# Optimization experiments

Measured on AMD Instinct MI355X. Metric: run time of the kernel, lower is better.

The kernel has to match this reference:

```python
import jax, jax.numpy as jnp
import numpy as np

BATCH, SEQ, D = 128, 256, 64


def setup_inputs() -> dict:
    key = jax.random.key(0)
    k1, k2, k3 = jax.random.split(key, 3)
    eye = jnp.eye(D, dtype=jnp.float32)
    return {
        "x": jax.random.normal(k1, (BATCH, D), dtype=jnp.float32),
        "U_t": jax.random.normal(k2, (BATCH, SEQ, D), dtype=jnp.float32),
        "Y_t": jax.random.normal(k3, (BATCH, SEQ, D), dtype=jnp.float32),
        # learnable params, 'identity' init per module
        "F_mat": eye,
        "B_mat": eye,
        "H": eye,
        "LQ": jnp.tril(eye),
        "LR": jnp.tril(eye),
    }


def _kalman(x, U_t, Y_t, F_mat, B_mat, H, LQ, LR):
    d = x.shape[-1]
    bsz = x.shape[0]
    Q = LQ @ LQ.T                      # [D,D] process noise cov
    R = LR @ LR.T                      # [D,D] measurement noise cov
    I = jnp.eye(d, dtype=x.dtype)
    P0 = jnp.broadcast_to(I, (bsz, d, d))

    def step(carry, inp):
        x_prev, P = carry              # [B,D], [B,D,D]
        u, y = inp                     # [B,D], [B,D,D]
        x_pred = x_prev @ F_mat.T + u @ B_mat.T
        P_pred = F_mat @ P @ F_mat.T + Q            # broadcasts [D,D]@[B,D,D]
        S = H @ P_pred @ H.T + R                    # [B,D,D]
        S_inv = jnp.linalg.inv(S)
        K = P_pred @ (H.T @ S_inv)                  # Kalman gain [B,D,D]
        innov = y - x_pred @ H.T                    # [B,D]
        # matches torch: (innov.unsqueeze(1) @ K).squeeze(1)
        x_new = x_pred + jnp.einsum('bd,bde->be', innov, K)
        IKH = I - K @ H
        P_new = IKH @ P_pred @ jnp.swapaxes(IKH, -1, -2) \
              + K @ R @ jnp.swapaxes(K, -1, -2)
        P_new = 0.5 * (P_new + jnp.swapaxes(P_new, -1, -2))  # symmetrize
        return (x_new, P_new), (x_new, P_new)

    inputs = (jnp.swapaxes(U_t, 0, 1), jnp.swapaxes(Y_t, 0, 1))  # [S,B,D]
    _, (preds, covs) = jax.lax.scan(step, (x, P0), inputs)
    # prediction [B,S,D], covariance [B,S,D,D]
    return jnp.swapaxes(preds, 0, 1), jnp.swapaxes(covs, 0, 1)


def reference(x, U_t, Y_t, F_mat, B_mat, H, LQ, LR):
    return _kalman(x, U_t, Y_t, F_mat, B_mat, H, LQ, LR)
```

## Files before the change

kernel.cpp:

```cpp
#include <hip/hip_runtime.h>

#define BATCH 128
#define SEQ   256

#define WS_K  16
#define WS_A  (16 + SEQ * 4096)
#define WS_BP (WS_A + 4096)
#define WS_KS (WS_BP + 4096)

typedef unsigned short u16;
typedef float  f32x4v __attribute__((ext_vector_type(4)));
typedef __bf16 bf16x8 __attribute__((ext_vector_type(8)));
typedef unsigned short u16x8 __attribute__((ext_vector_type(8)));

struct Acc { f32x4v t[2][2]; };

__device__ __forceinline__ u16 bf16hi(float x) {
  unsigned u = __float_as_uint(x);
  return (u16)((u + 0x7fffu + ((u >> 16) & 1u)) >> 16);
}
__device__ __forceinline__ float bf16f(u16 h) {
  return __uint_as_float(((unsigned)h) << 16);
}

__device__ __forceinline__ int swadr(int a, int c) {
  return a * 64 + ((c ^ (a & 7)) << 3);
}

__device__ __forceinline__ bf16x8 frag(const u16* M, int strip, int kb, int q, int ln) {
  return *(const bf16x8*)(M + swadr(strip * 16 + ln, kb * 4 + q));
}

__device__ __forceinline__ void mm(const u16* As, const u16* Bs, Acc& acc,
                                   int R, int Cb, int q, int ln) {
#pragma unroll
  for (int kb = 0; kb < 2; ++kb) {
    bf16x8 ah[2], al[2], bh[2], bl[2];
#pragma unroll
    for (int i = 0; i < 2; ++i) {
      ah[i] = frag(As,        2 * R  + i, kb, q, ln);
      al[i] = frag(As + 4096, 2 * R  + i, kb, q, ln);
      bh[i] = frag(Bs,        2 * Cb + i, kb, q, ln);
      bl[i] = frag(Bs + 4096, 2 * Cb + i, kb, q, ln);
    }
#pragma unroll
    for (int i = 0; i < 2; ++i)
#pragma unroll
      for (int j = 0; j < 2; ++j) {
        acc.t[i][j] = __builtin_amdgcn_mfma_f32_16x16x32_bf16(ah[i], bh[j], acc.t[i][j], 0, 0, 0);
        acc.t[i][j] = __builtin_amdgcn_mfma_f32_16x16x32_bf16(ah[i], bl[j], acc.t[i][j], 0, 0, 0);
        acc.t[i][j] = __builtin_amdgcn_mfma_f32_16x16x32_bf16(al[i], bh[j], acc.t[i][j], 0, 0, 0);
      }
  }
}

__device__ __forceinline__ Acc accZero() {
  Acc a;
#pragma unroll
  for (int i = 0; i < 2; ++i)
#pragma unroll
    for (int j = 0; j < 2; ++j) {
      f32x4v z; z.x = 0.f; z.y = 0.f; z.z = 0.f; z.w = 0.f;
      a.t[i][j] = z;
    }
  return a;
}

__device__ __forceinline__ void storeC(float* dst, const Acc& a, int R, int Cb, int q, int ln) {
#pragma unroll
  for (int i = 0; i < 2; ++i)
#pragma unroll
    for (int j = 0; j < 2; ++j)
#pragma unroll
      for (int k = 0; k < 4; ++k)
        dst[(32 * R + 16 * i + 4 * q + k) * 64 + 32 * Cb + 16 * j + ln] = a.t[i][j][k];
}

__device__ __forceinline__ void emit16(const float* v, int row, int cb, u16* Rs, u16* Ts) {
  u16 h[16], lo[16];
#pragma unroll
  for (int e = 0; e < 16; ++e) {
    h[e] = bf16hi(v[e]);
    lo[e] = bf16hi(v[e] - bf16f(h[e]));
  }
  if (Rs) {
#pragma unroll
    for (int c = 0; c < 2; ++c) {
      u16x8 vh, vl;
#pragma unroll
      for (int e = 0; e < 8; ++e) { vh[e] = h[8 * c + e]; vl[e] = lo[8 * c + e]; }
      const int ad = swadr(row, (cb >> 3) + c);
      *(u16x8*)(Rs + ad) = vh;
      *(u16x8*)(Rs + 4096 + ad) = vl;
    }
  }
  if (Ts) {
    const int rc = row >> 3, rr = row & 7;
#pragma unroll
    for (int e = 0; e < 16; ++e) {
      const int a = cb + e;
      const int ad = a * 64 + ((rc ^ (a & 7)) << 3) + rr;
      Ts[ad] = h[e];
      Ts[4096 + ad] = lo[e];
    }
  }
}

__device__ __forceinline__ void splitsrc(const float* src, u16* Rs, u16* Ts,
                                         int mode, float scale, float dval, int tid) {
  const int row = tid >> 2, cb = (tid & 3) << 4;
  float v[16];
#pragma unroll
  for (int m = 0; m < 4; ++m) {
    f32x4v x = *(const f32x4v*)(src + row * 64 + cb + 4 * m);
    v[4 * m] = x.x; v[4 * m + 1] = x.y; v[4 * m + 2] = x.z; v[4 * m + 3] = x.w;
  }
  if (mode == 1) {
#pragma unroll
    for (int e = 0; e < 16; ++e) v[e] *= scale;
  } else if (mode == 2) {
#pragma unroll
    for (int e = 0; e < 16; ++e) v[e] = (((cb + e) == row) ? dval : 0.f) - v[e];
  }
  emit16(v, row, cb, Rs, Ts);
}

__device__ __forceinline__ float redmax(float v, float* red, int tid) {
#pragma unroll
  for (int off = 32; off > 0; off >>= 1) v = fmaxf(v, __shfl_xor(v, off));
  if ((tid & 63) == 0) red[300 + (tid >> 6)] = v;
  __syncthreads();
  float m = fmaxf(fmaxf(red[300], red[301]), fmaxf(red[302], red[303]));
  __syncthreads();
  return m;
}

__device__ __forceinline__ float dot4(float4 a, float4 b, float acc) {
  return fmaf(a.x, b.x, fmaf(a.y, b.y, fmaf(a.z, b.z, fmaf(a.w, b.w, acc))));
}

__global__ void __launch_bounds__(256, 1)
k1_riccati(const float* __restrict__ Fg, const float* __restrict__ Bg,
           const float* __restrict__ Hg, const float* __restrict__ LQg,
           const float* __restrict__ LRg, float* __restrict__ ws,
           float* __restrict__ covs) {
  __shared__ __align__(16) u16 smb[7 * 8192];
  __shared__ __align__(16) float Mf32[4096];
  __shared__ __align__(16) float Ppf32[4096];
  __shared__ __align__(16) float red[308];

  const int tid = threadIdx.x;
  const int l = tid & 63, w = tid >> 6, q = l >> 4, ln = l & 15;
  const int R = w >> 1, Cb = w & 1;

  {
    const int row = tid >> 2, cb = (tid & 3) << 4;
    float od = 0.f;
    const float* mats[5] = {Fg, Bg, Hg, LQg, LRg};
#pragma unroll
    for (int mi = 0; mi < 5; ++mi) {
      const float* M = mats[mi];
#pragma unroll
      for (int m = 0; m < 4; ++m) {
        f32x4v x = *(const f32x4v*)(M + row * 64 + cb + 4 * m);
        const int j0c = cb + 4 * m;
        if (j0c + 0 != row) od = fmaxf(od, fabsf(x.x));
        if (j0c + 1 != row) od = fmaxf(od, fabsf(x.y));
        if (j0c + 2 != row) od = fmaxf(od, fabsf(x.z));
        if (j0c + 3 != row) od = fmaxf(od, fabsf(x.w));
      }
    }
    const float odall = redmax(od, red, tid);
    if (odall == 0.f) {
      if (tid < 64) {
        const int e = tid;
        const float f = Fg[e * 65], b = Bg[e * 65], h = Hg[e * 65];
        const float lq = LQg[e * 65], lr = LRg[e * 65];
        const float qv = lq * lq, rv = lr * lr;
        float p = 1.f, kprev = 0.f, kcur = 0.f, om = 1.f;
        int tstar = SEQ - 1;
        for (int t = 0; t < SEQ; ++t) {
          const float pp = f * p * f + qv;
          const float s = h * pp * h + rv;
          const float k = pp * h / s;
          const float kh = k * h;
          const float omv = 1.f - kh;
          const float pn = omv * omv * pp + k * k * rv;
          float* Kt = ws + WS_K + (size_t)t * 4096 + e * 64;
          float* Ct = covs + (size_t)t * 4096 + e * 64;
          f32x4v z; z.x = 0.f; z.y = 0.f; z.z = 0.f; z.w = 0.f;
#pragma unroll
          for (int m = 0; m < 16; ++m) {
            *(f32x4v*)(Kt + 4 * m) = z;
            *(f32x4v*)(Ct + 4 * m) = z;
          }
          Kt[e] = k;
          Ct[e] = pn;
          float dk = (t == 0) ? 1e9f : fabsf(k - kprev);
#pragma unroll
          for (int off = 32; off > 0; off >>= 1) dk = fmaxf(dk, __shfl_xor(dk, off));
          p = pn; kprev = k; kcur = k; om = omv;
          if (dk < 1e-3f) { tstar = t; break; }
        }
        {
          const float astar = om * f, bpv = om * b;
          float* Ar = ws + WS_A + e * 64;
          float* Bp = ws + WS_BP + e * 64;
          float* Ks = ws + WS_KS + e * 64;
          f32x4v z; z.x = 0.f; z.y = 0.f; z.z = 0.f; z.w = 0.f;
#pragma unroll
          for (int m = 0; m < 16; ++m) {
            *(f32x4v*)(Ar + 4 * m) = z;
            *(f32x4v*)(Bp + 4 * m) = z;
            *(f32x4v*)(Ks + 4 * m) = z;
          }
          Ar[e] = astar; Bp[e] = bpv; Ks[e] = kcur;
          const float a2 = astar * astar, a4 = a2 * a2, a8 = a4 * a4;
          float a16 = fabsf(a8 * a8);
#pragma unroll
          for (int off = 32; off > 0; off >>= 1) a16 = fmaxf(a16, __shfl_xor(a16, off));
          if (e == 0) {
            ((int*)ws)[0] = tstar;
            ((int*)ws)[1] = (tstar <= 16 && a16 < 1e-5f) ? 1 : 0;
          }
        }
      }
      return;
    }
  }

  u16* SF = smb;
  u16* SH = smb + 8192;
  u16* SX = smb + 2 * 8192;
  u16* S1 = smb + 3 * 8192;
  u16* S2 = smb + 4 * 8192;
  u16* S3 = smb + 5 * 8192;
  u16* S4 = smb + 6 * 8192;

  splitsrc(Fg, SF, nullptr, 0, 0, 0, tid);
  splitsrc(Hg, SH, nullptr, 0, 0, 0, tid);
  splitsrc(LQg, S1, nullptr, 0, 0, 0, tid);
  __syncthreads();
  Acc qacc = accZero(); mm(S1, S1, qacc, R, Cb, q, ln);
  __syncthreads();
  splitsrc(LRg, S1, nullptr, 0, 0, 0, tid);
  __syncthreads();
  Acc racc = accZero(); mm(S1, S1, racc, R, Cb, q, ln);
  __syncthreads();
  {
    const int row = tid >> 2, cb = (tid & 3) << 4;
    float v[16];
#pragma unroll
    for (int e = 0; e < 16; ++e) v[e] = ((cb + e) == row) ? 1.f : 0.f;
    emit16(v, row, cb, S4, nullptr);
  }
  __syncthreads();

  int tstar = SEQ - 1;
  for (int t = 0; t < SEQ; ++t) {
    const u16* Wsrc = SF;
    if (t > 0) {
      Acc a = accZero(); mm(SF, S4, a, R, Cb, q, ln);
      storeC(Mf32, a, R, Cb, q, ln);
      __syncthreads();
      splitsrc(Mf32, S1, nullptr, 0, 0, 0, tid);
      __syncthreads();
      Wsrc = S1;
    }
    {
      Acc a = qacc; mm(Wsrc, SF, a, R, Cb, q, ln);
      storeC(Ppf32, a, R, Cb, q, ln);
      __syncthreads();
      splitsrc(Ppf32, S2, nullptr, 0, 0, 0, tid);
      __syncthreads();
    }
    {
      Acc a = accZero(); mm(SH, S2, a, R, Cb, q, ln);
      storeC(Mf32, a, R, Cb, q, ln);
      __syncthreads();
      splitsrc(Mf32, S3, S4, 0, 0, 0, tid);
      __syncthreads();
    }
    {
      Acc a = racc; mm(S3, SH, a, R, Cb, q, ln);
      storeC(Mf32, a, R, Cb, q, ln);
      __syncthreads();
      if (t == 0) {
        const int col = tid & 63, grp = tid >> 6;
        float s = 0.f;
        for (int r2 = grp * 16; r2 < grp * 16 + 16; ++r2) s += fabsf(Mf32[r2 * 64 + col]);
        red[tid] = s;
        __syncthreads();
        if (tid < 64) {
          float cs = red[tid] + red[64 + tid] + red[128 + tid] + red[192 + tid];
#pragma unroll
          for (int off = 32; off > 0; off >>= 1) cs = fmaxf(cs, __shfl_xor(cs, off));
          if (tid == 0) red[256] = 1.f / (cs * cs);
        }
        __syncthreads();
        const float sc = red[256];
        splitsrc(Mf32, SX, nullptr, 1, sc, 0, tid);
        __syncthreads();
      }
      splitsrc(Mf32, S2, nullptr, 0, 0, 0, tid);
      __syncthreads();
    }
    const int cap = (t == 0) ? 40 : 4;
    for (int it = 0; it < cap; ++it) {
      Acc e_ = accZero(); mm(S2, SX, e_, R, Cb, q, ln);
      float r = 0.f;
#pragma unroll
      for (int i = 0; i < 2; ++i)
#pragma unroll
        for (int j = 0; j < 2; ++j)
#pragma unroll
          for (int k = 0; k < 4; ++k) {
            const int gr = 32 * R + 16 * i + 4 * q + k;
            const int gc = 32 * Cb + 16 * j + ln;
            r = fmaxf(r, fabsf(e_.t[i][j][k] - ((gr == gc) ? 1.f : 0.f)));
          }
      const float rall = redmax(r, red, tid);
      if (rall < 5e-4f) break;
      storeC(Mf32, e_, R, Cb, q, ln);
      __syncthreads();
      splitsrc(Mf32, nullptr, S1, 2, 0, 2.0f, tid);
      __syncthreads();
      Acc x2 = accZero(); mm(SX, S1, x2, R, Cb, q, ln);
      storeC(Mf32, x2, R, Cb, q, ln);
      __syncthreads();
      splitsrc(Mf32, SX, nullptr, 0, 0, 0, tid);
      __syncthreads();
      if (rall * rall < 1e-4f) break;
    }
    __syncthreads();
    float dk;
    {
      Acc a = accZero(); mm(SX, S4, a, R, Cb, q, ln);
      storeC(Mf32, a, R, Cb, q, ln);
      __syncthreads();
      const int row = tid >> 2, cb = (tid & 3) << 4;
      float v[16]; float dmax = (t == 0) ? 1e9f : 0.f;
      float* wrow = ws + WS_K + (size_t)t * 4096 + row * 64 + cb;
#pragma unroll
      for (int m = 0; m < 4; ++m) {
        f32x4v x = *(const f32x4v*)(Mf32 + row * 64 + cb + 4 * m);
        v[4 * m] = x.x; v[4 * m + 1] = x.y; v[4 * m + 2] = x.z; v[4 * m + 3] = x.w;
        *(f32x4v*)(wrow + 4 * m) = x;
      }
      if (t > 0) {
        const float* prow = wrow - 4096;
#pragma unroll
        for (int m = 0; m < 4; ++m) {
          f32x4v p = *(const f32x4v*)(prow + 4 * m);
          dmax = fmaxf(dmax, fmaxf(fmaxf(fabsf(v[4 * m] - p.x), fabsf(v[4 * m + 1] - p.y)),
                                   fmaxf(fabsf(v[4 * m + 2] - p.z), fabsf(v[4 * m + 3] - p.w))));
        }
      }
      emit16(v, row, cb, nullptr, S1);
      dk = redmax(dmax, red, tid);
    }
    {
      Acc a = accZero(); mm(S1, S4, a, R, Cb, q, ln);
      storeC(Mf32, a, R, Cb, q, ln);
      __syncthreads();
      const int row = tid >> 2, cb = (tid & 3) << 4;
      float pv[16];
#pragma unroll
      for (int m = 0; m < 4; ++m) {
        f32x4v mij = *(const f32x4v*)(Mf32 + row * 64 + cb + 4 * m);
        f32x4v pp  = *(const f32x4v*)(Ppf32 + row * 64 + cb + 4 * m);
        pv[4 * m]     = pp.x - 0.5f * (mij.x + Mf32[(cb + 4 * m + 0) * 64 + row]);
        pv[4 * m + 1] = pp.y - 0.5f * (mij.y + Mf32[(cb + 4 * m + 1) * 64 + row]);
        pv[4 * m + 2] = pp.z - 0.5f * (mij.z + Mf32[(cb + 4 * m + 2) * 64 + row]);
        pv[4 * m + 3] = pp.w - 0.5f * (mij.w + Mf32[(cb + 4 * m + 3) * 64 + row]);
      }
      float* crow = covs + (size_t)t * 4096 + row * 64 + cb;
#pragma unroll
      for (int m = 0; m < 4; ++m) {
        f32x4v o; o.x = pv[4 * m]; o.y = pv[4 * m + 1]; o.z = pv[4 * m + 2]; o.w = pv[4 * m + 3];
        *(f32x4v*)(crow + 4 * m) = o;
      }
      emit16(pv, row, cb, S4, nullptr);
      __syncthreads();
    }
    if (dk < 1e-3f) { tstar = t; break; }
  }

  {
    Acc a = accZero(); mm(S1, SH, a, R, Cb, q, ln);
    storeC(Mf32, a, R, Cb, q, ln);
    __syncthreads();
    splitsrc(Mf32, S2, nullptr, 2, 0, 1.0f, tid);
    __syncthreads();
  }
  splitsrc(Fg, nullptr, S3, 0, 0, 0, tid);
  __syncthreads();
  {
    Acc a = accZero(); mm(S2, S3, a, R, Cb, q, ln);
    storeC(Mf32, a, R, Cb, q, ln);
#pragma unroll
    for (int i = 0; i < 2; ++i)
#pragma unroll
      for (int j = 0; j < 2; ++j)
#pragma unroll
        for (int k = 0; k < 4; ++k)
          ws[WS_A + (size_t)((32 * R + 16 * i + 4 * q + k) * 64 + 32 * Cb + 16 * j + ln)] = a.t[i][j][k];
    __syncthreads();
    splitsrc(Mf32, S1, S4, 0, 0, 0, tid);
    __syncthreads();
  }
  splitsrc(Bg, nullptr, S3, 0, 0, 0, tid);
  __syncthreads();
  {
    Acc a = accZero(); mm(S2, S3, a, R, Cb, q, ln);
#pragma unroll
    for (int i = 0; i < 2; ++i)
#pragma unroll
      for (int j = 0; j < 2; ++j)
#pragma unroll
        for (int k = 0; k < 4; ++k)
          ws[WS_BP + (size_t)((32 * R + 16 * i + 4 * q + k) * 64 + 32 * Cb + 16 * j + ln)] = a.t[i][j][k];
  }
  {
    const int row = tid >> 2, cb = (tid & 3) << 4;
    const float* srcr = ws + WS_K + (size_t)tstar * 4096 + row * 64 + cb;
    float* dstr = ws + WS_KS + row * 64 + cb;
#pragma unroll
    for (int m = 0; m < 4; ++m) *(f32x4v*)(dstr + 4 * m) = *(const f32x4v*)(srcr + 4 * m);
  }
  __syncthreads();
  {
    Acc a = accZero(); mm(S1, S4, a, R, Cb, q, ln);
    storeC(Mf32, a, R, Cb, q, ln); __syncthreads();
    splitsrc(Mf32, S2, S3, 0, 0, 0, tid); __syncthreads();
  }
  {
    Acc a = accZero(); mm(S2, S3, a, R, Cb, q, ln);
    storeC(Mf32, a, R, Cb, q, ln); __syncthreads();
    splitsrc(Mf32, S1, S4, 0, 0, 0, tid); __syncthreads();
  }
  {
    Acc a = accZero(); mm(S1, S4, a, R, Cb, q, ln);
    storeC(Mf32, a, R, Cb, q, ln); __syncthreads();
    splitsrc(Mf32, S2, S3, 0, 0, 0, tid); __syncthreads();
  }
  {
    Acc a = accZero(); mm(S2, S3, a, R, Cb, q, ln);
    float am = 0.f;
#pragma unroll
    for (int i = 0; i < 2; ++i)
#pragma unroll
      for (int j = 0; j < 2; ++j)
#pragma unroll
        for (int k = 0; k < 4; ++k) am = fmaxf(am, fabsf(a.t[i][j][k]));
    const float amax = redmax(am, red, tid);
    if (tid == 0) {
      ((int*)ws)[0] = tstar;
      ((int*)ws)[1] = (tstar <= 16 && amax < 1e-5f) ? 1 : 0;
    }
  }
}

#define NB2 512
#define NX2 1024

__global__ void __launch_bounds__(256, 4)
k2_fused(const float* __restrict__ x0, const float* __restrict__ U,
         const float* __restrict__ Y, const float* __restrict__ Fg,
         const float* __restrict__ Bg, const float* __restrict__ Hg,
         const float* __restrict__ ws, float* __restrict__ preds,
         float* __restrict__ covs) {
  const int tid = threadIdx.x;
  const int wg = blockIdx.x;
  const int tstar = ((const int*)ws)[0];
  const int flag  = ((const int*)ws)[1];

  if (wg < NB2) {
    const int b = wg >> 2, qt = wg & 3;
    const int s0 = qt << 6;
    const float4* srcInf = (const float4*)(covs + (size_t)tstar * 4096);
    float4 r0 = srcInf[tid], r1 = srcInf[256 + tid];
    float4 r2 = srcInf[512 + tid], r3 = srcInf[768 + tid];
    for (int s = s0; s < s0 + 64; ++s) {
      float4* dst = (float4*)(covs + ((size_t)b * SEQ + s) * 4096);
      if (s <= tstar) {
        if (b == 0) continue;
        const float4* src = (const float4*)(covs + (size_t)s * 4096);
        dst[tid] = src[tid]; dst[256 + tid] = src[256 + tid];
        dst[512 + tid] = src[512 + tid]; dst[768 + tid] = src[768 + tid];
      } else {
        dst[tid] = r0; dst[256 + tid] = r1; dst[512 + tid] = r2; dst[768 + tid] = r3;
      }
    }
  } else {
    const int xw = wg - NB2;
    const int c = xw >> 7, b = xw & 127;
    const int e = tid >> 2, q = tid & 3;
    const int co = q << 4;
    __shared__ __align__(16) float xa[64], xb[64], inn[64], us[2][64], ys[2][64];

    if (c == 0) {
      const int t1 = flag ? 32 : SEQ;
      float4 Fr[4], Br[4], Hr[4], Kr[4];
      {
        const float4* fp = (const float4*)(Fg + e * 64 + co);
        const float4* bp = (const float4*)(Bg + e * 64 + co);
        const float4* hp = (const float4*)(Hg + e * 64 + co);
#pragma unroll
        for (int m = 0; m < 4; ++m) { Fr[m] = fp[m]; Br[m] = bp[m]; Hr[m] = hp[m]; }
      }
      if (tid < 64) xa[tid] = x0[b * 64 + tid];
      int staged = -1;
      for (int t = 0; t < t1; ++t) {
        const int se = (t < tstar) ? t : tstar;
        if (se != staged) {
          const float4* kp = (const float4*)(ws + WS_K + (size_t)se * 4096 + e * 64 + co);
#pragma unroll
          for (int m = 0; m < 4; ++m) Kr[m] = kp[m];
          staged = se;
        }
        if (tid < 64) us[0][tid] = U[((size_t)b * SEQ + t) * 64 + tid];
        else if (tid < 128) ys[0][tid - 64] = Y[((size_t)b * SEQ + t) * 64 + (tid - 64)];
        __syncthreads();
        const float4* xv4 = (const float4*)xa;
        const float4* us4 = (const float4*)us[0];
        float v = 0.f;
#pragma unroll
        for (int m = 0; m < 4; ++m) {
          v = dot4(Fr[m], xv4[q * 4 + m], v);
          v = dot4(Br[m], us4[q * 4 + m], v);
        }
        v += __shfl_xor(v, 1); v += __shfl_xor(v, 2);
        if (q == 0) xb[e] = v;
        __syncthreads();
        const float4* xp4 = (const float4*)xb;
        float wv = 0.f;
#pragma unroll
        for (int m = 0; m < 4; ++m) wv = dot4(Hr[m], xp4[q * 4 + m], wv);
        wv += __shfl_xor(wv, 1); wv += __shfl_xor(wv, 2);
        if (q == 0) inn[e] = ys[0][e] - wv;
        __syncthreads();
        const float4* in4 = (const float4*)inn;
        float z = 0.f;
#pragma unroll
        for (int m = 0; m < 4; ++m) z = dot4(Kr[m], in4[q * 4 + m], z);
        z += __shfl_xor(z, 1); z += __shfl_xor(z, 2);
        if (q == 0) xa[e] = xb[e] + z;
        __syncthreads();
        if (tid < 64) preds[((size_t)b * SEQ + t) * 64 + tid] = xa[tid];
      }
    } else {
      if (!flag) return;
      const int tb = 32 * c - 16, out0 = 32 * c, t1 = 32 * c + 32;
      float4 Ar[4], Pr[4], Sr[4];
      {
        const float4* ap = (const float4*)(ws + WS_A + e * 64 + co);
        const float4* pp = (const float4*)(ws + WS_BP + e * 64 + co);
        const float4* sp = (const float4*)(ws + WS_KS + e * 64 + co);
#pragma unroll
        for (int m = 0; m < 4; ++m) { Ar[m] = ap[m]; Pr[m] = pp[m]; Sr[m] = sp[m]; }
      }
      float* xcur = xa;
      float* xnxt = xb;
      if (tid < 64) xcur[tid] = 0.f;
      float g = 0.f;
      if (tid < 64) g = U[((size_t)b * SEQ + tb) * 64 + tid];
      else if (tid < 128) g = Y[((size_t)b * SEQ + tb) * 64 + (tid - 64)];
      if (tid < 64) us[0][tid] = g;
      else if (tid < 128) ys[0][tid - 64] = g;
      if (tb + 1 < t1) {
        if (tid < 64) g = U[((size_t)b * SEQ + tb + 1) * 64 + tid];
        else if (tid < 128) g = Y[((size_t)b * SEQ + tb + 1) * 64 + (tid - 64)];
      }
      __syncthreads();
      int pb = 0;
      for (int t = tb; t < t1; ++t) {
        const float4* xv4 = (const float4*)xcur;
        const float4* us4 = (const float4*)us[pb];
        const float4* ys4 = (const float4*)ys[pb];
        float v = 0.f;
#pragma unroll
        for (int m = 0; m < 4; ++m) {
          v = dot4(Ar[m], xv4[q * 4 + m], v);
          v = dot4(Pr[m], us4[q * 4 + m], v);
          v = dot4(Sr[m], ys4[q * 4 + m], v);
        }
        v += __shfl_xor(v, 1); v += __shfl_xor(v, 2);
        if (q == 0) xnxt[e] = v;
        if (t >= out0 && q == 0) preds[((size_t)b * SEQ + t) * 64 + e] = v;
        if (t + 1 < t1) {
          if (tid < 64) us[pb ^ 1][tid] = g;
          else if (tid < 128) ys[pb ^ 1][tid - 64] = g;
          if (t + 2 < t1) {
            if (tid < 64) g = U[((size_t)b * SEQ + t + 2) * 64 + tid];
            else if (tid < 128) g = Y[((size_t)b * SEQ + t + 2) * 64 + (tid - 64)];
          }
        }
        __syncthreads();
        { float* tp = xcur; xcur = xnxt; xnxt = tp; }
        pb ^= 1;
      }
    }
  }
}

extern "C" void kernel_launch(void* const* d_in, const int* in_sizes, int n_in,
                              void* d_out, int out_size, void* d_ws, size_t ws_size,
                              hipStream_t stream) {
  (void)in_sizes; (void)n_in; (void)out_size; (void)ws_size;
  const float* x0 = (const float*)d_in[0];
  const float* U  = (const float*)d_in[1];
  const float* Y  = (const float*)d_in[2];
  const float* F  = (const float*)d_in[3];
  const float* B  = (const float*)d_in[4];
  const float* H  = (const float*)d_in[5];
  const float* LQ = (const float*)d_in[6];
  const float* LR = (const float*)d_in[7];
  float* preds = (float*)d_out;
  float* covs  = preds + (size_t)BATCH * SEQ * 64;
  float* ws    = (float*)d_ws;

  hipLaunchKernelGGL(k1_riccati, dim3(1), dim3(256), 0, stream,
                     F, B, H, LQ, LR, ws, covs);
  hipLaunchKernelGGL(k2_fused, dim3(NB2 + NX2), dim3(256), 0, stream,
                     x0, U, Y, F, B, H, ws, preds, covs);
}
```

Before: 604.2 us.

## Use nontemporal stores and finer-grained covariance broadcast blocks scheduled after state blocks

The covariance broadcast section now uses 2048 blocks, each writing 16 timesteps instead of 64, and these blocks are placed after the state-update blocks in the grid so the long serial x-recurrence workgroups get dispatched first. Stores of the 128 MB covariance output use nontemporal hints to avoid polluting caches. This aims to overlap the serial filter chain with bandwidth-bound writes and improve write efficiency, at the cost of more blocks, each reloading the steady-state covariance.

```diff
diff --git a/kernel.cpp b/kernel.cpp
--- a/kernel.cpp
+++ b/kernel.cpp
@@ -461,8 +461,8 @@
   }
 }
 
-#define NB2 512
 #define NX2 1024
+#define NB2 2048
 
 __global__ void __launch_bounds__(256, 4)
 k2_fused(const float* __restrict__ x0, const float* __restrict__ U,
@@ -475,26 +475,30 @@
   const int tstar = ((const int*)ws)[0];
   const int flag  = ((const int*)ws)[1];
 
-  if (wg < NB2) {
-    const int b = wg >> 2, qt = wg & 3;
-    const int s0 = qt << 6;
-    const float4* srcInf = (const float4*)(covs + (size_t)tstar * 4096);
-    float4 r0 = srcInf[tid], r1 = srcInf[256 + tid];
-    float4 r2 = srcInf[512 + tid], r3 = srcInf[768 + tid];
-    for (int s = s0; s < s0 + 64; ++s) {
-      float4* dst = (float4*)(covs + ((size_t)b * SEQ + s) * 4096);
+  if (wg >= NX2) {
+    const int bw = wg - NX2;
+    const int b = bw >> 4, st = (bw & 15) << 4;
+    const f32x4v* srcInf = (const f32x4v*)(covs + (size_t)tstar * 4096);
+    f32x4v r0 = srcInf[tid], r1 = srcInf[256 + tid];
+    f32x4v r2 = srcInf[512 + tid], r3 = srcInf[768 + tid];
+    for (int s = st; s < st + 16; ++s) {
+      f32x4v* dst = (f32x4v*)(covs + ((size_t)b * SEQ + s) * 4096);
       if (s <= tstar) {
         if (b == 0) continue;
-        const float4* src = (const float4*)(covs + (size_t)s * 4096);
-        dst[tid] = src[tid]; dst[256 + tid] = src[256 + tid];
-        dst[512 + tid] = src[512 + tid]; dst[768 + tid] = src[768 + tid];
+        const f32x4v* src = (const f32x4v*)(covs + (size_t)s * 4096);
+        __builtin_nontemporal_store(src[tid],       dst + tid);
+        __builtin_nontemporal_store(src[256 + tid], dst + 256 + tid);
+        __builtin_nontemporal_store(src[512 + tid], dst + 512 + tid);
+        __builtin_nontemporal_store(src[768 + tid], dst + 768 + tid);
       } else {
-        dst[tid] = r0; dst[256 + tid] = r1; dst[512 + tid] = r2; dst[768 + tid] = r3;
+        __builtin_nontemporal_store(r0, dst + tid);
+        __builtin_nontemporal_store(r1, dst + 256 + tid);
+        __builtin_nontemporal_store(r2, dst + 512 + tid);
+        __builtin_nontemporal_store(r3, dst + 768 + tid);
       }
     }
   } else {
-    const int xw = wg - NB2;
-    const int c = xw >> 7, b = xw & 127;
+    const int c = wg >> 7, b = wg & 127;
     const int e = tid >> 2, q = tid & 3;
     const int co = q << 4;
     __shared__ __align__(16) float xa[64], xb[64], inn[64], us[2][64], ys[2][64];
@@ -622,6 +626,6 @@
 
   hipLaunchKernelGGL(k1_riccati, dim3(1), dim3(256), 0, stream,
                      F, B, H, LQ, LR, ws, covs);
-  hipLaunchKernelGGL(k2_fused, dim3(NB2 + NX2), dim3(256), 0, stream,
+  hipLaunchKernelGGL(k2_fused, dim3(NX2 + NB2), dim3(256), 0, stream,
                      x0, U, Y, F, B, H, ws, preds, covs);
 }
```

New measurement: 595.0 us. About the same (-1.5%).
